# Kernel optimization log

Hardware: AMD Instinct MI355X
Metric: run time of the kernel (lower is better)

Reference implementation:

```python
import jax, jax.numpy as jnp
import numpy as np

DIM = 768
HEADS = 12
HEAD_DIM = DIM // HEADS
NUM_CLASSES = 1000
SCALE = HEAD_DIM ** (-0.5)


def setup_inputs() -> dict:
    key = jax.random.key(0)
    ks = jax.random.split(key, 6)
    B, N = 4, 2048
    s = 0.02
    return {
        "x": jax.random.normal(ks[0], (B, N, DIM), dtype=jnp.float32),
        "w_qkv": jax.random.normal(ks[1], (DIM, 3 * DIM), dtype=jnp.float32) * s,
        "w_proj": jax.random.normal(ks[2], (DIM, DIM), dtype=jnp.float32) * s,
        "b_proj": jax.random.normal(ks[3], (DIM,), dtype=jnp.float32) * s,
        "w_head": jax.random.normal(ks[4], (DIM, NUM_CLASSES), dtype=jnp.float32) * s,
        "b_head": jax.random.normal(ks[5], (NUM_CLASSES,), dtype=jnp.float32) * s,
    }


def reference(x, w_qkv, w_proj, b_proj, w_head, b_head):
    B, N, C = x.shape
    qkv = (x @ w_qkv).reshape(B, N, 3, HEADS, HEAD_DIM)
    qkv = jnp.transpose(qkv, (2, 0, 3, 1, 4))  # [3, B, H, N, hd]
    q, k, v = qkv[0], qkv[1], qkv[2]
    attn = jnp.einsum("bhnd,bhmd->bhnm", q, k) * SCALE  # [B,H,N,N]
    attn = jax.nn.softmax(attn, axis=-1)
    out = jnp.einsum("bhnm,bhmd->bhnd", attn, v)  # [B,H,N,hd]
    out = jnp.transpose(out, (0, 2, 1, 3)).reshape(B, N, C)
    out = out @ w_proj + b_proj
    out = out @ w_head + b_head  # [B,N,num_classes]
    return jnp.max(out, axis=1)  # [B,num_classes]
```

## Files before the change

kernel.cpp:

```cpp
#include <hip/hip_runtime.h>
#include <hip/hip_bf16.h>

typedef __attribute__((ext_vector_type(8))) short short8;
typedef __attribute__((ext_vector_type(4))) float f32x4;
typedef __attribute__((ext_vector_type(16))) float f32x16;
typedef unsigned short u16t;
typedef unsigned int u32t;

#define MFMA16(a, b, c) __builtin_amdgcn_mfma_f32_16x16x32_bf16((a), (b), (c), 0, 0, 0)
#define MFMA32(a, b, c) __builtin_amdgcn_mfma_f32_32x32x16_bf16((a), (b), (c), 0, 0, 0)

__device__ __forceinline__ u16t f2b(float f) {
    union { float f; u32t u; } v; v.f = f;
    u32t u = v.u + 0x7FFFu + ((v.u >> 16) & 1u);
    return (u16t)(u >> 16);
}
__device__ __forceinline__ u32t encf(float f) {
    union { float f; u32t u; } v; v.f = f;
    return (v.u & 0x80000000u) ? ~v.u : (v.u | 0x80000000u);
}
__device__ __forceinline__ float decf(u32t u) {
    union { u32t u; float f; } v;
    v.u = (u & 0x80000000u) ? (u ^ 0x80000000u) : ~u;
    return v.f;
}
__device__ __forceinline__ float fexp2(float x) {
#if __has_builtin(__builtin_amdgcn_exp2f)
    return __builtin_amdgcn_exp2f(x);
#else
    return __expf(x * 0.6931471805599453f);
#endif
}
__device__ __forceinline__ void gload16(const u16t* g, u16t* l) {
    __builtin_amdgcn_global_load_lds((const __attribute__((address_space(1))) void*)g,
                                     (__attribute__((address_space(3))) void*)l, 16, 0, 0);
}

__global__ __launch_bounds__(256) void k_prolog(const float* __restrict__ x, u16t* __restrict__ xb,
                                                const float* __restrict__ wp, u16t* __restrict__ wpb,
                                                const float* __restrict__ Wq, u16t* __restrict__ WqT,
                                                const float* __restrict__ Wh, u16t* __restrict__ WhT) {
    int bid = blockIdx.x;
    int tid = threadIdx.x;
    if (bid < 6720) {
        const float* src; u16t* dst; int i;
        if (bid < 6144) { src = x;  dst = xb;  i = bid * 256 + tid; }
        else            { src = wp; dst = wpb; i = (bid - 6144) * 256 + tid; }
        float4 v = ((const float4*)src)[i];
        ushort4 o;
        o.x = f2b(v.x); o.y = f2b(v.y); o.z = f2b(v.z); o.w = f2b(v.w);
        ((ushort4*)dst)[i] = o;
    } else {
        __shared__ float t[32][33];
        const float* W; u16t* WT; int N, NP, n0, k0;
        if (bid < 8448) {
            int local = bid - 6720;
            W = Wq; WT = WqT; N = 2304; NP = 2304;
            n0 = (local % 72) * 32; k0 = (local / 72) * 32;
        } else {
            int local = bid - 8448;
            W = Wh; WT = WhT; N = 1000; NP = 1024;
            n0 = (local % 32) * 32; k0 = (local / 32) * 32;
        }
        const int K = 768;
        int tx = tid & 31, ty = tid >> 5;
        for (int i = 0; i < 32; i += 8) {
            int k = k0 + ty + i, n = n0 + tx;
            t[ty + i][tx] = (n < N) ? W[(size_t)k * N + n] : 0.f;
        }
        __syncthreads();
        for (int i = 0; i < 32; i += 8) {
            int n = n0 + ty + i, k = k0 + tx;
            if (n < NP) WT[(size_t)n * K + k] = f2b(t[tx][ty + i]);
        }
    }
}

__global__ __launch_bounds__(256) void k_decode_out(u32t* __restrict__ o, int n) {
    int i = blockIdx.x * 256 + threadIdx.x;
    if (i < n) {
        float f = decf(o[i]);
        ((float*)o)[i] = f;
    }
}

#define BM 128
#define BN 128

#define QSCALE 0.18033688011112042f

template <int EPI>
__device__ __forceinline__ void gemm_core(u16t* As, u16t* Bs,
                                          const u16t* __restrict__ A, const u16t* __restrict__ BT,
                                          int M, int N, int K,
                                          u16t* __restrict__ Cb, const float* __restrict__ bias,
                                          u32t* __restrict__ omax, int wg) {
    int tid = threadIdx.x;
    int lane = tid & 63, wid = tid >> 6;
    int wr = wid >> 1, wc = wid & 1;
    int g = lane >> 4, l15 = lane & 15;

    int nx = N >> 7;
    int bx = wg % nx, by = wg / nx;
    int m0 = by * BM, n0 = bx * BN;

    f32x4 acc[4][4];
    for (int i = 0; i < 4; i++)
        for (int j = 0; j < 4; j++) acc[i][j] = (f32x4){0.f, 0.f, 0.f, 0.f};

    const u16t* pa[4]; const u16t* pb[4]; u16t* da[4]; u16t* db[4];
#pragma unroll
    for (int i = 0; i < 4; i++) {
        int c = tid + 256 * i;
        int row = (c >> 2) & 127;
        int kcol = (c >> 9) * 32 + (c & 3) * 8;
        pa[i] = A + (size_t)(m0 + row) * K + kcol;
        pb[i] = BT + (size_t)(n0 + row) * K + kcol;
        da[i] = &As[c * 8];
        db[i] = &Bs[c * 8];
    }

    auto stage = [&](int buf, int k0) {
        int boff = buf * (BM * 64);
#pragma unroll
        for (int i = 0; i < 4; i++) gload16(pa[i] + k0, da[i] + boff);
#pragma unroll
        for (int i = 0; i < 4; i++) gload16(pb[i] + k0, db[i] + boff);
    };

    const int NT = K >> 6;
    stage(0, 0);

#pragma unroll 1
    for (int t = 0; t < NT; ++t) {
        const int cur = t & 1;
        if (t + 1 < NT) {
            stage(cur ^ 1, (t + 1) << 6);
            asm volatile("s_waitcnt vmcnt(8)" ::: "memory");
        } else {
            asm volatile("s_waitcnt vmcnt(0)" ::: "memory");
        }
        __builtin_amdgcn_s_barrier();

        const u16t* Ab = &As[cur * (BM * 64)];
        const u16t* Bb = &Bs[cur * (BN * 64)];
#pragma unroll
        for (int kk = 0; kk < 2; kk++) {
            short8 af[4], bf[4];
#pragma unroll
            for (int i = 0; i < 4; i++) af[i] = *(const short8*)&Ab[kk * 4096 + (wr * 64 + i * 16 + l15) * 32 + g * 8];
#pragma unroll
            for (int j = 0; j < 4; j++) bf[j] = *(const short8*)&Bb[kk * 4096 + (wc * 64 + j * 16 + l15) * 32 + g * 8];
#pragma unroll
            for (int i = 0; i < 4; i++)
#pragma unroll
                for (int j = 0; j < 4; j++) acc[i][j] = MFMA16(af[i], bf[j], acc[i][j]);
        }
        asm volatile("s_waitcnt lgkmcnt(0)" ::: "memory");
        __builtin_amdgcn_s_barrier();
    }

    if constexpr (EPI == 0) {
        for (int i = 0; i < 4; i++)
            for (int j = 0; j < 4; j++)
                for (int r = 0; r < 4; r++) {
                    int row = m0 + wr * 64 + i * 16 + g * 4 + r;
                    int col = n0 + wc * 64 + j * 16 + l15;
                    int t = col / 768, rem = col - t * 768;
                    int hh = rem >> 6, d = rem & 63;
                    int bb = row >> 11, n = row & 2047;
                    float v = acc[i][j][r];
                    size_t idx;
                    if (t == 0) {
                        v *= QSCALE;
                        idx = ((size_t)(bb * 12 + hh)) * 131072 + (size_t)n * 64 + d;
                    } else if (t == 1) {
                        idx = ((size_t)(48 + bb * 12 + hh)) * 131072 + (size_t)n * 64 + d;
                    } else {
                        int np = (n & ~12) | ((n & 4) << 1) | ((n & 8) >> 1);
                        idx = ((size_t)(96 + bb * 12 + hh)) * 131072 + (size_t)d * 2048 + np;
                    }
                    Cb[idx] = f2b(v);
                }
    } else if constexpr (EPI == 3) {
        for (int i = 0; i < 4; i++)
            for (int j = 0; j < 4; j++)
                for (int r = 0; r < 4; r++) {
                    int row = m0 + wr * 64 + i * 16 + g * 4 + r;
                    int col = n0 + wc * 64 + j * 16 + l15;
                    Cb[(size_t)row * N + col] = f2b(acc[i][j][r]);
                }
    } else {
        float* smax = (float*)As;
        float cmax[4];
        for (int j = 0; j < 4; j++) {
            float m = -3.0e38f;
            for (int i = 0; i < 4; i++)
                for (int r = 0; r < 4; r++) m = fmaxf(m, acc[i][j][r]);
            m = fmaxf(m, __shfl_xor(m, 16));
            m = fmaxf(m, __shfl_xor(m, 32));
            cmax[j] = m;
        }
        __syncthreads();
        if (lane < 16)
            for (int j = 0; j < 4; j++) smax[wr * BN + wc * 64 + j * 16 + lane] = cmax[j];
        __syncthreads();
        if (tid < BN) {
            int col = n0 + tid;
            if (col < 1000) {
                float m = fmaxf(smax[tid], smax[BN + tid]) + bias[col];
                int b = m0 >> 11;
                atomicMax(&omax[b * 1000 + col], encf(m));
            }
        }
    }
}

__global__ __launch_bounds__(256) void k_mega(const u16t* __restrict__ xb, const u16t* __restrict__ wqkvT,
                                              u16t* __restrict__ qkv,
                                              const u16t* __restrict__ wheadT, const u16t* __restrict__ wprojb,
                                              u16t* __restrict__ WfT,
                                              const float* __restrict__ bproj, const float* __restrict__ whead,
                                              const float* __restrict__ bhead, float* __restrict__ bias_f,
                                              u32t* __restrict__ outb) {
    __shared__ alignas(16) u16t As[2 * BM * 64];
    __shared__ alignas(16) u16t Bs[2 * BN * 64];
    int bid = blockIdx.x;
    if (bid < 1152) {
        int wg = (bid & 7) * 144 + (bid >> 3);
        gemm_core<0>(As, Bs, xb, wqkvT, 8192, 2304, 768, qkv, nullptr, nullptr, wg);
    } else if (bid < 1200) {
        int q = bid - 1152;
        int wg = (q & 7) * 6 + (q >> 3);
        gemm_core<3>(As, Bs, wheadT, wprojb, 1024, 768, 768, WfT, nullptr, nullptr, wg);
    } else if (bid < 1264) {
        float* red = (float*)As;
        int t = threadIdx.x;
        int c = t & 15;
        int jg = t >> 4;
        int blk = bid - 1200;
        int n = blk * 16 + c;
        float s = 0.f;
        if (n < 1000) {
#pragma unroll 4
            for (int j = jg * 48; j < jg * 48 + 48; ++j)
                s += bproj[j] * whead[j * 1000 + n];
        }
        red[t] = s;
        __syncthreads();
        for (int off = 128; off >= 16; off >>= 1) {
            if (t < off) red[t] += red[t + off];
            __syncthreads();
        }
        if (t < 16) {
            int nn = blk * 16 + t;
            bias_f[nn] = (nn < 1000) ? (red[t] + bhead[nn]) : 0.f;
        }
    } else {
        int i = (bid - 1264) * 256 + threadIdx.x;
        if (i < 4000) outb[i] = 0u;
    }
}

__global__ __launch_bounds__(256) void k_gemm_fin(const u16t* __restrict__ A, const u16t* __restrict__ BT,
                                                  const float* __restrict__ bias, u32t* __restrict__ omax) {
    __shared__ alignas(16) u16t As[2 * BM * 64];
    __shared__ alignas(16) u16t Bs[2 * BN * 64];
    int bid = blockIdx.x;
    int wg = (bid & 7) * 64 + (bid >> 3);
    gemm_core<2>(As, Bs, A, BT, 8192, 1024, 768, nullptr, bias, omax, wg);
}

__global__ __launch_bounds__(256) void k_flash(const u16t* __restrict__ QKV, u16t* __restrict__ AO) {
    __shared__ alignas(16) u16t Kc[3][4096];
    __shared__ alignas(16) u16t Vc[3][4096];

    const int tid = threadIdx.x;
    const int lane = tid & 63;
    const int h = lane >> 5;
    const int l31 = lane & 31;
    const int w = tid >> 6;
    const int wk = ((blockIdx.x & 7) * 96) + (blockIdx.x >> 3);
    const int qt = wk & 15;
    const int hb = wk >> 4;
    const int head = hb % 12, b = hb / 12;
    const u16t* Qg = QKV + ((size_t)hb) * 131072;
    const u16t* Kg = QKV + ((size_t)(48 + hb)) * 131072;
    const u16t* Vg = QKV + ((size_t)(96 + hb)) * 131072;
    const int q0w = qt * 128 + w * 32;

    short8 qf[4];
#pragma unroll
    for (int ks = 0; ks < 4; ++ks)
        qf[ks] = *(const short8*)&Qg[(size_t)(q0w + l31) * 64 + ks * 16 + h * 8];
    asm volatile("s_waitcnt vmcnt(0)" ::: "memory");

    short8 vone;
#pragma unroll
    for (int e = 0; e < 8; ++e) vone[e] = (short)0x3F80;

    f32x16 o0, o1, lsum, fz;
#pragma unroll
    for (int r = 0; r < 16; ++r) { o0[r] = 0.f; o1[r] = 0.f; lsum[r] = 0.f; fz[r] = 0.f; }
    asm volatile("" : "+v"(fz));

    auto stage = [&](int bi, int kv0) {
#pragma unroll
        for (int c = 0; c < 2; ++c) {
            int ic = c * 256 + tid;
            int ss = ic >> 8, ks = (ic >> 6) & 3, l6 = ic & 63;
            int hh = l6 >> 5, lq = l6 & 31;
            const u16t* gs = Kg + ((size_t)(kv0 + ss * 32 + lq) << 6) + ks * 16 + hh * 8;
            gload16(gs, &Kc[bi][ic * 8]);
        }
#pragma unroll
        for (int c = 0; c < 2; ++c) {
            int ic = c * 256 + tid;
            int jb = ic >> 8, ks = (ic >> 6) & 3, l6 = ic & 63;
            int hh = l6 >> 5, ld = l6 & 31;
            const u16t* gs = Vg + (size_t)(jb * 32 + ld) * 2048 + kv0 + ks * 16 + hh * 8;
            gload16(gs, &Vc[bi][ic * 8]);
        }
    };

    stage(0, 0);
    stage(1, 64);

#pragma unroll 1
    for (int t = 0; t < 32; ++t) {
        const int cur = t % 3;
        if (t < 30) {
            stage((t + 2) % 3, (t + 2) * 64);
            asm volatile("s_waitcnt vmcnt(8)" ::: "memory");
        } else if (t == 30) {
            asm volatile("s_waitcnt vmcnt(4)" ::: "memory");
        } else {
            asm volatile("s_waitcnt vmcnt(0)" ::: "memory");
        }
        __builtin_amdgcn_s_barrier();

        const u16t* Kb = &Kc[cur][0];
        const u16t* Vb = &Vc[cur][0];

        f32x16 s0, s1;
        __builtin_amdgcn_s_setprio(1);
        {
            short8 k0 = *(const short8*)&Kb[(0 * 64 + lane) * 8];
            short8 k1 = *(const short8*)&Kb[(4 * 64 + lane) * 8];
            s0 = MFMA32(k0, qf[0], fz);
            s1 = MFMA32(k1, qf[0], fz);
        }
#pragma unroll
        for (int ks = 1; ks < 4; ++ks) {
            short8 k0 = *(const short8*)&Kb[(ks * 64 + lane) * 8];
            short8 k1 = *(const short8*)&Kb[((4 + ks) * 64 + lane) * 8];
            s0 = MFMA32(k0, qf[ks], s0);
            s1 = MFMA32(k1, qf[ks], s1);
        }
        __builtin_amdgcn_s_setprio(0);

        short8 pf[4];
        auto packhalf = [&](const f32x16& sv, int half, int idx) {
            union { u32t wu[4]; short8 v; } u;
#pragma unroll
            for (int wq = 0; wq < 4; ++wq) {
                float lo = fexp2(sv[half * 8 + 2 * wq]);
                float hi = fexp2(sv[half * 8 + 2 * wq + 1]);
                asm("v_cvt_pk_bf16_f32 %0, %1, %2" : "=v"(u.wu[wq]) : "v"(lo), "v"(hi));
            }
            pf[idx] = u.v;
        };
        packhalf(s0, 0, 0);
        packhalf(s0, 1, 1);
        packhalf(s1, 0, 2);
        packhalf(s1, 1, 3);

        __builtin_amdgcn_s_setprio(1);
#pragma unroll
        for (int ks = 0; ks < 4; ++ks) {
            short8 v0 = *(const short8*)&Vb[(ks * 64 + lane) * 8];
            short8 v1 = *(const short8*)&Vb[((4 + ks) * 64 + lane) * 8];
            o0 = MFMA32(pf[ks], v0, o0);
            o1 = MFMA32(pf[ks], v1, o1);
            lsum = MFMA32(pf[ks], vone, lsum);
        }
        __builtin_amdgcn_s_setprio(0);

        asm volatile("s_waitcnt lgkmcnt(0)" ::: "memory");
        __builtin_amdgcn_s_barrier();
    }

#pragma unroll
    for (int r = 0; r < 16; ++r) {
        int q = (r & 3) + 8 * (r >> 2) + 4 * h;
        float rn = 1.0f / lsum[r];
        u16t* dst = AO + (size_t)(b * 2048 + q0w + q) * 768 + head * 64;
        dst[l31] = f2b(o0[r] * rn);
        dst[32 + l31] = f2b(o1[r] * rn);
    }
}

extern "C" void kernel_launch(void* const* d_in, const int* in_sizes, int n_in,
                              void* d_out, int out_size, void* d_ws, size_t ws_size,
                              hipStream_t stream) {
    const float* x = (const float*)d_in[0];
    const float* w_qkv = (const float*)d_in[1];
    const float* w_proj = (const float*)d_in[2];
    const float* b_proj = (const float*)d_in[3];
    const float* w_head = (const float*)d_in[4];
    const float* b_head = (const float*)d_in[5];

    char* ws = (char*)d_ws;
    u16t* xb = (u16t*)(ws);
    u16t* wqkvT = (u16t*)(ws + 12582912);
    u16t* wheadT = (u16t*)(ws + 16121856);
    u16t* wprojb = (u16t*)(ws + 17694720);
    u16t* qkv = (u16t*)(ws + 18874368);
    u16t* ao = (u16t*)(ws + 56623104);
    u16t* WfT = (u16t*)(ws + 69206016);
    float* bias_f = (float*)(ws + 70778880);

    k_prolog<<<9216, 256, 0, stream>>>(x, xb, w_proj, wprojb, w_qkv, wqkvT, w_head, wheadT);
    k_mega<<<1280, 256, 0, stream>>>(xb, wqkvT, qkv, wheadT, wprojb, WfT,
                                     b_proj, w_head, b_head, bias_f, (u32t*)d_out);
    k_flash<<<768, 256, 0, stream>>>(qkv, ao);
    k_gemm_fin<<<512, 256, 0, stream>>>(ao, WfT, bias_f, (u32t*)d_out);
    k_decode_out<<<16, 256, 0, stream>>>((u32t*)d_out, 4000);
}
```

Baseline: 170.7 us.

## Fuse x fp32-to-bf16 conversion into QKV GEMM and fold output decode into final GEMM

Removes the separate pass that converts x to bf16. The QKV GEMM now loads fp32 x directly into registers, converts it with packed bf16 instructions and writes the result to LDS, with register prefetch overlapping the MFMA work. It also drops the decode kernel: the last-finishing block of the final GEMM, detected through an atomic counter, decodes the output in place. This saves an HBM round trip of x in bf16 and one kernel launch, at the cost of more register pressure and doubled A-load bandwidth inside the GEMM.

```diff
diff --git a/kernel.cpp b/kernel.cpp
--- a/kernel.cpp
+++ b/kernel.cpp
@@ -36,29 +36,26 @@
                                      (__attribute__((address_space(3))) void*)l, 16, 0, 0);
 }
 
-__global__ __launch_bounds__(256) void k_prolog(const float* __restrict__ x, u16t* __restrict__ xb,
-                                                const float* __restrict__ wp, u16t* __restrict__ wpb,
+__global__ __launch_bounds__(256) void k_prolog(const float* __restrict__ wp, u16t* __restrict__ wpb,
                                                 const float* __restrict__ Wq, u16t* __restrict__ WqT,
                                                 const float* __restrict__ Wh, u16t* __restrict__ WhT) {
     int bid = blockIdx.x;
     int tid = threadIdx.x;
-    if (bid < 6720) {
-        const float* src; u16t* dst; int i;
-        if (bid < 6144) { src = x;  dst = xb;  i = bid * 256 + tid; }
-        else            { src = wp; dst = wpb; i = (bid - 6144) * 256 + tid; }
-        float4 v = ((const float4*)src)[i];
+    if (bid < 576) {
+        int i = bid * 256 + tid;
+        float4 v = ((const float4*)wp)[i];
         ushort4 o;
         o.x = f2b(v.x); o.y = f2b(v.y); o.z = f2b(v.z); o.w = f2b(v.w);
-        ((ushort4*)dst)[i] = o;
+        ((ushort4*)wpb)[i] = o;
     } else {
         __shared__ float t[32][33];
         const float* W; u16t* WT; int N, NP, n0, k0;
-        if (bid < 8448) {
-            int local = bid - 6720;
+        if (bid < 2304) {
+            int local = bid - 576;
             W = Wq; WT = WqT; N = 2304; NP = 2304;
             n0 = (local % 72) * 32; k0 = (local / 72) * 32;
         } else {
-            int local = bid - 8448;
+            int local = bid - 2304;
             W = Wh; WT = WhT; N = 1000; NP = 1024;
             n0 = (local % 32) * 32; k0 = (local / 32) * 32;
         }
@@ -73,14 +70,6 @@
             int n = n0 + ty + i, k = k0 + tx;
             if (n < NP) WT[(size_t)n * K + k] = f2b(t[tx][ty + i]);
         }
-    }
-}
-
-__global__ __launch_bounds__(256) void k_decode_out(u32t* __restrict__ o, int n) {
-    int i = blockIdx.x * 256 + threadIdx.x;
-    if (i < n) {
-        float f = decf(o[i]);
-        ((float*)o)[i] = f;
     }
 }
 
@@ -160,29 +149,7 @@
         __builtin_amdgcn_s_barrier();
     }
 
-    if constexpr (EPI == 0) {
-        for (int i = 0; i < 4; i++)
-            for (int j = 0; j < 4; j++)
-                for (int r = 0; r < 4; r++) {
-                    int row = m0 + wr * 64 + i * 16 + g * 4 + r;
-                    int col = n0 + wc * 64 + j * 16 + l15;
-                    int t = col / 768, rem = col - t * 768;
-                    int hh = rem >> 6, d = rem & 63;
-                    int bb = row >> 11, n = row & 2047;
-                    float v = acc[i][j][r];
-                    size_t idx;
-                    if (t == 0) {
-                        v *= QSCALE;
-                        idx = ((size_t)(bb * 12 + hh)) * 131072 + (size_t)n * 64 + d;
-                    } else if (t == 1) {
-                        idx = ((size_t)(48 + bb * 12 + hh)) * 131072 + (size_t)n * 64 + d;
-                    } else {
-                        int np = (n & ~12) | ((n & 4) << 1) | ((n & 8) >> 1);
-                        idx = ((size_t)(96 + bb * 12 + hh)) * 131072 + (size_t)d * 2048 + np;
-                    }
-                    Cb[idx] = f2b(v);
-                }
-    } else if constexpr (EPI == 3) {
+    if constexpr (EPI == 3) {
         for (int i = 0; i < 4; i++)
             for (int j = 0; j < 4; j++)
                 for (int r = 0; r < 4; r++) {
@@ -216,19 +183,138 @@
     }
 }
 
-__global__ __launch_bounds__(256) void k_mega(const u16t* __restrict__ xb, const u16t* __restrict__ wqkvT,
+__device__ __forceinline__ void qkv_core_f32A(u16t* As, u16t* Bs,
+                                              const float* __restrict__ A, const u16t* __restrict__ BT,
+                                              u16t* __restrict__ Cb, int wg) {
+    const int K = 768;
+    int tid = threadIdx.x;
+    int lane = tid & 63, wid = tid >> 6;
+    int wr = wid >> 1, wc = wid & 1;
+    int g = lane >> 4, l15 = lane & 15;
+
+    int bx = wg % 18, by = wg / 18;
+    int m0 = by * BM, n0 = bx * BN;
+
+    f32x4 acc[4][4];
+    for (int i = 0; i < 4; i++)
+        for (int j = 0; j < 4; j++) acc[i][j] = (f32x4){0.f, 0.f, 0.f, 0.f};
+
+    const float* pa[4]; const u16t* pb[4]; u16t* da[4]; u16t* db[4];
+#pragma unroll
+    for (int i = 0; i < 4; i++) {
+        int c = tid + 256 * i;
+        int row = (c >> 2) & 127;
+        int kcol = (c >> 9) * 32 + (c & 3) * 8;
+        pa[i] = A + (size_t)(m0 + row) * K + kcol;
+        pb[i] = BT + (size_t)(n0 + row) * K + kcol;
+        da[i] = &As[c * 8];
+        db[i] = &Bs[c * 8];
+    }
+
+    float4 ra[4][2];
+
+    auto loadA = [&](int ko) {
+#pragma unroll
+        for (int i = 0; i < 4; i++) {
+            ra[i][0] = *(const float4*)(pa[i] + ko);
+            ra[i][1] = *(const float4*)(pa[i] + ko + 4);
+        }
+    };
+    auto cvtWriteA = [&](int boff) {
+#pragma unroll
+        for (int i = 0; i < 4; i++) {
+            union { u32t w[4]; short8 v; } u;
+            asm("v_cvt_pk_bf16_f32 %0, %1, %2" : "=v"(u.w[0]) : "v"(ra[i][0].x), "v"(ra[i][0].y));
+            asm("v_cvt_pk_bf16_f32 %0, %1, %2" : "=v"(u.w[1]) : "v"(ra[i][0].z), "v"(ra[i][0].w));
+            asm("v_cvt_pk_bf16_f32 %0, %1, %2" : "=v"(u.w[2]) : "v"(ra[i][1].x), "v"(ra[i][1].y));
+            asm("v_cvt_pk_bf16_f32 %0, %1, %2" : "=v"(u.w[3]) : "v"(ra[i][1].z), "v"(ra[i][1].w));
+            *(short8*)(da[i] + boff) = u.v;
+        }
+    };
+    auto stageB = [&](int buf, int ko) {
+        int boff = buf * (BN * 64);
+#pragma unroll
+        for (int i = 0; i < 4; i++) gload16(pb[i] + ko, db[i] + boff);
+    };
+
+    const int NT = K >> 6;
+
+    loadA(0);
+    asm volatile("s_waitcnt vmcnt(0)" ::: "memory");
+    cvtWriteA(0);
+    asm volatile("s_waitcnt lgkmcnt(0)" ::: "memory");
+    stageB(0, 0);
+
+#pragma unroll 1
+    for (int t = 0; t < NT; ++t) {
+        const int cur = t & 1;
+        if (t + 1 < NT) {
+            loadA((t + 1) << 6);
+            stageB(cur ^ 1, (t + 1) << 6);
+            asm volatile("s_waitcnt vmcnt(12)" ::: "memory");
+        } else {
+            asm volatile("s_waitcnt vmcnt(0)" ::: "memory");
+        }
+        __builtin_amdgcn_s_barrier();
+
+        const u16t* Ab = &As[cur * (BM * 64)];
+        const u16t* Bb = &Bs[cur * (BN * 64)];
+#pragma unroll
+        for (int kk = 0; kk < 2; kk++) {
+            short8 af[4], bf[4];
+#pragma unroll
+            for (int i = 0; i < 4; i++) af[i] = *(const short8*)&Ab[kk * 4096 + (wr * 64 + i * 16 + l15) * 32 + g * 8];
+#pragma unroll
+            for (int j = 0; j < 4; j++) bf[j] = *(const short8*)&Bb[kk * 4096 + (wc * 64 + j * 16 + l15) * 32 + g * 8];
+#pragma unroll
+            for (int i = 0; i < 4; i++)
+#pragma unroll
+                for (int j = 0; j < 4; j++) acc[i][j] = MFMA16(af[i], bf[j], acc[i][j]);
+        }
+        if (t + 1 < NT) {
+            asm volatile("s_waitcnt vmcnt(4)" ::: "memory");
+            cvtWriteA((cur ^ 1) * (BM * 64));
+        }
+        asm volatile("s_waitcnt lgkmcnt(0)" ::: "memory");
+        __builtin_amdgcn_s_barrier();
+    }
+
+    for (int i = 0; i < 4; i++)
+        for (int j = 0; j < 4; j++)
+            for (int r = 0; r < 4; r++) {
+                int row = m0 + wr * 64 + i * 16 + g * 4 + r;
+                int col = n0 + wc * 64 + j * 16 + l15;
+                int t = col / 768, rem = col - t * 768;
+                int hh = rem >> 6, d = rem & 63;
+                int bb = row >> 11, n = row & 2047;
+                float v = acc[i][j][r];
+                size_t idx;
+                if (t == 0) {
+                    v *= QSCALE;
+                    idx = ((size_t)(bb * 12 + hh)) * 131072 + (size_t)n * 64 + d;
+                } else if (t == 1) {
+                    idx = ((size_t)(48 + bb * 12 + hh)) * 131072 + (size_t)n * 64 + d;
+                } else {
+                    int np = (n & ~12) | ((n & 4) << 1) | ((n & 8) >> 1);
+                    idx = ((size_t)(96 + bb * 12 + hh)) * 131072 + (size_t)d * 2048 + np;
+                }
+                Cb[idx] = f2b(v);
+            }
+}
+
+__global__ __launch_bounds__(256) void k_mega(const float* __restrict__ x, const u16t* __restrict__ wqkvT,
                                               u16t* __restrict__ qkv,
                                               const u16t* __restrict__ wheadT, const u16t* __restrict__ wprojb,
                                               u16t* __restrict__ WfT,
                                               const float* __restrict__ bproj, const float* __restrict__ whead,
                                               const float* __restrict__ bhead, float* __restrict__ bias_f,
-                                              u32t* __restrict__ outb) {
+                                              u32t* __restrict__ outb, u32t* __restrict__ counter) {
     __shared__ alignas(16) u16t As[2 * BM * 64];
     __shared__ alignas(16) u16t Bs[2 * BN * 64];
     int bid = blockIdx.x;
     if (bid < 1152) {
         int wg = (bid & 7) * 144 + (bid >> 3);
-        gemm_core<0>(As, Bs, xb, wqkvT, 8192, 2304, 768, qkv, nullptr, nullptr, wg);
+        qkv_core_f32A(As, Bs, x, wqkvT, qkv, wg);
     } else if (bid < 1200) {
         int q = bid - 1152;
         int wg = (q & 7) * 6 + (q >> 3);
@@ -259,16 +345,31 @@
     } else {
         int i = (bid - 1264) * 256 + threadIdx.x;
         if (i < 4000) outb[i] = 0u;
+        else if (i == 4000) *counter = 0u;
     }
 }
 
 __global__ __launch_bounds__(256) void k_gemm_fin(const u16t* __restrict__ A, const u16t* __restrict__ BT,
-                                                  const float* __restrict__ bias, u32t* __restrict__ omax) {
+                                                  const float* __restrict__ bias, u32t* __restrict__ omax,
+                                                  u32t* __restrict__ counter) {
     __shared__ alignas(16) u16t As[2 * BM * 64];
     __shared__ alignas(16) u16t Bs[2 * BN * 64];
+    __shared__ u32t lastflag;
     int bid = blockIdx.x;
     int wg = (bid & 7) * 64 + (bid >> 3);
     gemm_core<2>(As, Bs, A, BT, 8192, 1024, 768, nullptr, bias, omax, wg);
+
+    __threadfence();
+    __syncthreads();
+    if (threadIdx.x == 0) lastflag = (atomicAdd(counter, 1u) == 511u) ? 1u : 0u;
+    __syncthreads();
+    if (lastflag) {
+        __threadfence();
+        for (int i = threadIdx.x; i < 4000; i += 256) {
+            u32t e = atomicMax(&omax[i], 0u);
+            ((float*)omax)[i] = decf(e);
+        }
+    }
 }
 
 __global__ __launch_bounds__(256) void k_flash(const u16t* __restrict__ QKV, u16t* __restrict__ AO) {
@@ -411,7 +512,6 @@
     const float* b_head = (const float*)d_in[5];
 
     char* ws = (char*)d_ws;
-    u16t* xb = (u16t*)(ws);
     u16t* wqkvT = (u16t*)(ws + 12582912);
     u16t* wheadT = (u16t*)(ws + 16121856);
     u16t* wprojb = (u16t*)(ws + 17694720);
@@ -419,11 +519,11 @@
     u16t* ao = (u16t*)(ws + 56623104);
     u16t* WfT = (u16t*)(ws + 69206016);
     float* bias_f = (float*)(ws + 70778880);
-
-    k_prolog<<<9216, 256, 0, stream>>>(x, xb, w_proj, wprojb, w_qkv, wqkvT, w_head, wheadT);
-    k_mega<<<1280, 256, 0, stream>>>(xb, wqkvT, qkv, wheadT, wprojb, WfT,
-                                     b_proj, w_head, b_head, bias_f, (u32t*)d_out);
+    u32t* counter = (u32t*)(ws + 70782976);
+
+    k_prolog<<<3072, 256, 0, stream>>>(w_proj, wprojb, w_qkv, wqkvT, w_head, wheadT);
+    k_mega<<<1280, 256, 0, stream>>>(x, wqkvT, qkv, wheadT, wprojb, WfT,
+                                     b_proj, w_head, b_head, bias_f, (u32t*)d_out, counter);
     k_flash<<<768, 256, 0, stream>>>(qkv, ao);
-    k_gemm_fin<<<512, 256, 0, stream>>>(ao, WfT, bias_f, (u32t*)d_out);
-    k_decode_out<<<16, 256, 0, stream>>>((u32t*)d_out, 4000);
-}
+    k_gemm_fin<<<512, 256, 0, stream>>>(ao, WfT, bias_f, (u32t*)d_out, counter);
+}
```

New measurement: 207.8 us. 21.7% more time.
